# Performance work log

Hardware: AMD Instinct MI355X
Metric: run time of the kernel (lower is better)

The kernel has to match this reference:

```python
import jax, jax.numpy as jnp
import numpy as np

B, N, F_IN, K, OUT = 64, 512, 6, 8, 3
SLOPE = 0.01  # torch LeakyReLU default negative_slope


def lrelu(x):
    return jnp.where(x >= 0, x, SLOPE * x)


def edge_mlp(e, w1, b1, w2, b2):
    # Linear -> LeakyReLU -> Linear -> LeakyReLU (EdgeConvMLP / mlp1)
    return lrelu(lrelu(e @ w1 + b1) @ w2 + b2)


def dyn_edge_conv(x, w1, b1, w2, b2):
    # x: [B, N, F]. kNN in feature space within each graph (self included,
    # matching torch_cluster.knn used by PyG DynamicEdgeConv).
    x2 = jnp.sum(x * x, -1)                                   # [B, N]
    d = x2[:, :, None] + x2[:, None, :] - 2.0 * jnp.einsum('bnf,bmf->bnm', x, x)
    idx = jax.lax.top_k(-d, K)[1]                              # [B, N, K]
    xj = jax.vmap(lambda xb, ib: xb[ib])(x, idx)               # [B, N, K, F]
    xi = jnp.broadcast_to(x[:, :, None, :], xj.shape)
    e = jnp.concatenate([xi, xj - xi], -1)                     # [B, N, K, 2F]
    h = edge_mlp(e, w1, b1, w2, b2)                            # [B, N, K, 256]
    return h.max(axis=2)                                       # max aggregation


def _lin(key, din, dout):
    kw, kb = jax.random.split(key)
    s = 1.0 / np.sqrt(din)
    w = jax.random.uniform(kw, (din, dout), jnp.float32, -s, s)
    b = jax.random.uniform(kb, (dout,), jnp.float32, -s, s)
    return w, b


def setup_inputs() -> dict:
    key = jax.random.key(0)
    ks = jax.random.split(key, 20)
    inp = {}
    inp['x'] = jax.random.normal(ks[0], (B * N, F_IN), jnp.float32)
    inp['edge_index'] = jax.random.randint(ks[1], (2, B * N * K), 0, B * N, jnp.int64)  # unused
    inp['batch'] = jnp.repeat(jnp.arange(B, dtype=jnp.int64), N)
    dims = [(2 * F_IN, 336, 256), (512, 336, 256), (512, 336, 256), (512, 336, 256)]
    for i, (din, dh, do) in enumerate(dims):
        w1, b1 = _lin(ks[2 + 2 * i], din, dh)
        w2, b2 = _lin(ks[3 + 2 * i], dh, do)
        inp[f'c{i+1}_w1'], inp[f'c{i+1}_b1'] = w1, b1
        inp[f'c{i+1}_w2'], inp[f'c{i+1}_b2'] = w2, b2
    inp['m1_w1'], inp['m1_b1'] = _lin(ks[10], 256 * 4 + F_IN, 336)
    inp['m1_w2'], inp['m1_b2'] = _lin(ks[11], 336, 256)
    inp['m2_w1'], inp['m2_b1'] = _lin(ks[12], 256, 128)
    inp['m2_w2'], inp['m2_b2'] = _lin(ks[13], 128, OUT)
    return inp


def reference(x, edge_index, batch,
              c1_w1, c1_b1, c1_w2, c1_b2,
              c2_w1, c2_b1, c2_w2, c2_b2,
              c3_w1, c3_b1, c3_w2, c3_b2,
              c4_w1, c4_b1, c4_w2, c4_b2,
              m1_w1, m1_b1, m1_w2, m1_b2,
              m2_w1, m2_b1, m2_w2, m2_b2):
    # edge_index is unused: DynamicEdgeConv rebuilds the kNN graph each layer.
    # Equal-sized graphs: reshape instead of segment ops (batch = repeat(arange(B), N)).
    xb = x.reshape(B, N, F_IN)
    x1 = dyn_edge_conv(xb, c1_w1, c1_b1, c1_w2, c1_b2)
    x2 = dyn_edge_conv(x1, c2_w1, c2_b1, c2_w2, c2_b2)
    x3 = dyn_edge_conv(x2, c3_w1, c3_b1, c3_w2, c3_b2)
    x4 = dyn_edge_conv(x3, c4_w1, c4_b1, c4_w2, c4_b2)
    h = jnp.concatenate([xb, x1, x2, x3, x4], -1)   # [B, N, 1030]
    h = edge_mlp(h, m1_w1, m1_b1, m1_w2, m1_b2)     # [B, N, 256]
    g = h.mean(axis=1)                              # global_mean_pool -> [B, 256]
    return lrelu(g @ m2_w1 + m2_b1) @ m2_w2 + m2_b2  # [B, OUT]
```

## Files before the change

### kernel.cpp

```cpp
#include <hip/hip_runtime.h>
#include <hip/hip_bf16.h>


#define DEVFN __device__ __forceinline__
DEVFN float lrelu(float v) { return v >= 0.f ? v : 0.01f * v; }

using bf16x8 = __attribute__((ext_vector_type(8))) short;
using f32x4  = __attribute__((ext_vector_type(4))) float;

template<int N> struct IC { static constexpr int value = N; };

DEVFN unsigned short f2bf(float v) {
    __hip_bfloat16 h = __float2bfloat16(v);
    return *(unsigned short*)&h;
}
DEVFN float bf2f(unsigned short u) {
    return __uint_as_float((unsigned)u << 16);
}

struct PDesc { const float* src; unsigned short* dst; int Kt, NT, N, mode, p0, p1, Ksrc; };
struct PTable { PDesc d[13]; };

__global__ __launch_bounds__(256) void pack_kernel(PTable tb) {
    PDesc d = tb.d[blockIdx.y];
    int i = blockIdx.x * 256 + threadIdx.x;
    int tot = d.Kt * d.NT * 512;
    if (i >= tot) return;
    int j = i & 7, lane = (i >> 3) & 63;
    int tile = i >> 9;
    int nt = tile % d.NT, kt = tile / d.NT;
    int k = kt * 32 + ((lane >> 4) << 3) + j;
    int n = nt * 16 + (lane & 15);
    float v = 0.f;
    if (d.mode == 0) {
        if (k < d.Ksrc) v = d.src[(size_t)k * d.N + n];
    } else if (d.mode == 1) {
        if (k < d.p1) v = d.src[(size_t)k * d.N + n] - d.src[(size_t)(k + d.p1) * d.N + n];
        else if (k >= d.p0 && k < d.p0 + d.p1) v = d.src[(size_t)(k - d.p0 + d.p1) * d.N + n];
    } else if (d.mode == 2) {
        if (k < 6) v = d.src[(size_t)k * d.N + n];
        else if (k >= 32 && k < 1056) v = d.src[(size_t)(k - 26) * d.N + n];
    } else {
        v = d.src[(size_t)(k + d.p0) * d.N + n];
    }
    d.dst[i] = f2bf(v);
}

__global__ __launch_bounds__(256) void xbprep_kernel(const float* __restrict__ xb,
                                                     unsigned short* __restrict__ xbbf,
                                                     unsigned short* __restrict__ xcat) {
    int p = blockIdx.x * 256 + threadIdx.x;
    if (p >= 32768) return;
    unsigned short r[16];
    #pragma unroll
    for (int c = 0; c < 6; ++c) r[c] = f2bf(xb[p * 6 + c]);
    #pragma unroll
    for (int c = 6; c < 16; ++c) r[c] = 0;
    #pragma unroll
    for (int c = 0; c < 16; ++c) xbbf[p * 16 + c] = r[c];
    unsigned short* xc = xcat + (size_t)p * 1056;
    #pragma unroll
    for (int c = 0; c < 16; ++c) xc[c] = r[c];
    #pragma unroll
    for (int c = 16; c < 32; ++c) xc[c] = 0;
}

template<int F>
__global__ __launch_bounds__(256) void norms_kernel(const float* __restrict__ f,
                                                    float* __restrict__ nrm) {
    int p = blockIdx.x * 256 + threadIdx.x;
    if (p >= 64 * 512) return;
    const float* r = f + (size_t)p * F;
    float s = 0.f;
    #pragma unroll
    for (int i = 0; i < F; ++i) s += r[i] * r[i];
    nrm[p] = s;
}

template<int F>
__global__ __launch_bounds__(256) void knn_kernel(const float* __restrict__ feat,
                                                  const float* __restrict__ nrm,
                                                  int* __restrict__ knn) {
    constexpr int FP = (F == 6) ? 8 : (F + 4);
    __shared__ float Xq[32 * FP];
    __shared__ float Xc[32 * FP];
    __shared__ float qn[32], cn[32];
    __shared__ float dt[32 * 33];
    const int t  = threadIdx.x;
    const int b  = blockIdx.x >> 4;
    const int n0 = (blockIdx.x & 15) << 5;
    const float* fg = feat + (size_t)b * 512 * F;

    for (int i = t; i < 32 * F; i += 256) {
        int r = i / F, c = i - r * F;
        Xq[r * FP + c] = fg[(size_t)(n0 + r) * F + c];
    }
    if (t < 32) qn[t] = nrm[b * 512 + n0 + t];

    float d8[8]; int i8[8];
    #pragma unroll
    for (int k = 0; k < 8; ++k) { d8[k] = 3.4e38f; i8[k] = 0; }

    const int q = t >> 3, cs = t & 7;

    for (int ct = 0; ct < 16; ++ct) {
        const int c0 = ct << 5;
        __syncthreads();
        for (int i = t; i < 32 * F; i += 256) {
            int r = i / F, c = i - r * F;
            Xc[r * FP + c] = fg[(size_t)(c0 + r) * F + c];
        }
        if (t < 32) cn[t] = nrm[b * 512 + c0 + t];
        __syncthreads();

        float acc[4] = {0.f, 0.f, 0.f, 0.f};
        #pragma unroll
        for (int f = 0; f < F; ++f) {
            float qv = Xq[q * FP + f];
            #pragma unroll
            for (int j = 0; j < 4; ++j) acc[j] += qv * Xc[(cs + 8 * j) * FP + f];
        }
        #pragma unroll
        for (int j = 0; j < 4; ++j)
            dt[q * 33 + cs + 8 * j] = qn[q] + cn[cs + 8 * j] - 2.f * acc[j];
        __syncthreads();

        if (t < 32) {
            #pragma unroll 1
            for (int i = 0; i < 32; ++i) {
                float d = dt[t * 33 + i];
                if (d < d8[7]) {
                    d8[7] = d; i8[7] = c0 + i;
                    #pragma unroll
                    for (int s = 7; s >= 1; --s) {
                        if (d8[s] < d8[s - 1]) {
                            float td = d8[s]; d8[s] = d8[s - 1]; d8[s - 1] = td;
                            int   ti = i8[s]; i8[s] = i8[s - 1]; i8[s - 1] = ti;
                        }
                    }
                }
            }
        }
    }
    if (t < 32) {
        #pragma unroll
        for (int k = 0; k < 8; ++k)
            knn[((size_t)b * 512 + n0 + t) * 8 + k] = i8[k];
    }
}

__global__ __launch_bounds__(256, 2)
void knn_mfma(const unsigned short* __restrict__ xfl,
              const float* __restrict__ nrm,
              int* __restrict__ knn) {
    __shared__ unsigned short Qh[64 * 72], Ql[64 * 72], Ch[64 * 72], Cl[64 * 72];
    __shared__ float dt[64 * 66];
    __shared__ float qn[64], cn[64];
    float* mD = dt;
    int*   mI = (int*)(dt + 2048);

    const int t  = threadIdx.x;
    const int l  = t & 63, w = t >> 6;
    const int m16 = l & 15, q4 = l >> 4;
    const int bx = blockIdx.x;
    const int slot = bx >> 3;
    const int b  = (bx & 7) + 8 * (slot >> 3);
    const int qs = (slot & 7) << 6;

    if (t < 64) qn[t] = nrm[b * 512 + qs + t];

    float d8[8]; int i8[8];
    #pragma unroll
    for (int k = 0; k < 8; ++k) { d8[k] = 3.4e38f; i8[k] = 0x7fffffff; }

    const int sr = t >> 2;
    const int sc = (t & 3) << 4;
    const int tq = t & 63, sub = t >> 6;

    for (int cs = 0; cs < 8; ++cs) {
        const int c0 = cs << 6;
        if (t < 64) cn[t] = nrm[b * 512 + c0 + t];

        f32x4 acc[4];
        #pragma unroll
        for (int i = 0; i < 4; ++i) acc[i] = (f32x4){0.f, 0.f, 0.f, 0.f};

        for (int kc = 0; kc < 4; ++kc) {
            const int k0 = kc << 6;
            __syncthreads();
            {
                const unsigned short* qr = xfl + (size_t)(b * 512 + qs + sr) * 512;
                const unsigned short* cr = xfl + (size_t)(b * 512 + c0 + sr) * 512;
                *(uint4*)&Qh[sr * 72 + sc]     = *(const uint4*)(qr + k0 + sc);
                *(uint4*)&Qh[sr * 72 + sc + 8] = *(const uint4*)(qr + k0 + sc + 8);
                *(uint4*)&Ql[sr * 72 + sc]     = *(const uint4*)(qr + 256 + k0 + sc);
                *(uint4*)&Ql[sr * 72 + sc + 8] = *(const uint4*)(qr + 256 + k0 + sc + 8);
                *(uint4*)&Ch[sr * 72 + sc]     = *(const uint4*)(cr + k0 + sc);
                *(uint4*)&Ch[sr * 72 + sc + 8] = *(const uint4*)(cr + k0 + sc + 8);
                *(uint4*)&Cl[sr * 72 + sc]     = *(const uint4*)(cr + 256 + k0 + sc);
                *(uint4*)&Cl[sr * 72 + sc + 8] = *(const uint4*)(cr + 256 + k0 + sc + 8);
            }
            __syncthreads();

            #pragma unroll
            for (int kt = 0; kt < 2; ++kt) {
                const int ko = kt * 32 + q4 * 8;
                bf16x8 ah = *(const bf16x8*)&Qh[(w * 16 + m16) * 72 + ko];
                bf16x8 al = *(const bf16x8*)&Ql[(w * 16 + m16) * 72 + ko];
                #pragma unroll
                for (int nt = 0; nt < 4; ++nt) {
                    bf16x8 bh = *(const bf16x8*)&Ch[(nt * 16 + m16) * 72 + ko];
                    bf16x8 bl = *(const bf16x8*)&Cl[(nt * 16 + m16) * 72 + ko];
                    acc[nt] = __builtin_amdgcn_mfma_f32_16x16x32_bf16(ah, bh, acc[nt], 0, 0, 0);
                    acc[nt] = __builtin_amdgcn_mfma_f32_16x16x32_bf16(ah, bl, acc[nt], 0, 0, 0);
                    acc[nt] = __builtin_amdgcn_mfma_f32_16x16x32_bf16(al, bh, acc[nt], 0, 0, 0);
                }
            }
        }

        #pragma unroll
        for (int nt = 0; nt < 4; ++nt) {
            float cv = cn[nt * 16 + m16];
            #pragma unroll
            for (int rr = 0; rr < 4; ++rr) {
                int qr = w * 16 + q4 * 4 + rr;
                dt[qr * 66 + nt * 16 + m16] = qn[qr] + cv - 2.f * acc[nt][rr];
            }
        }
        __syncthreads();

        {
            const float* drow = &dt[tq * 66 + sub * 16];
            #pragma unroll 1
            for (int j = 0; j < 16; ++j) {
                float d = drow[j];
                if (d < d8[7]) {
                    d8[7] = d; i8[7] = c0 + sub * 16 + j;
                    #pragma unroll
                    for (int s = 7; s >= 1; --s) {
                        if (d8[s] < d8[s - 1]) {
                            float td = d8[s]; d8[s] = d8[s - 1]; d8[s - 1] = td;
                            int   ti = i8[s]; i8[s] = i8[s - 1]; i8[s - 1] = ti;
                        }
                    }
                }
            }
        }
        __syncthreads();
    }

    #pragma unroll
    for (int k = 0; k < 8; ++k) {
        mD[(tq * 4 + sub) * 8 + k] = d8[k];
        mI[(tq * 4 + sub) * 8 + k] = i8[k];
    }
    __syncthreads();
    if (t < 64) {
        int p[4] = {0, 0, 0, 0};
        int outb = (b * 512 + qs + t) * 8;
        #pragma unroll 1
        for (int k = 0; k < 8; ++k) {
            float bd = 3.5e38f; int bi = 0x7fffffff; int bs = 0;
            #pragma unroll
            for (int s = 0; s < 4; ++s) {
                if (p[s] < 8) {
                    float dd = mD[(t * 4 + s) * 8 + p[s]];
                    int   ii = mI[(t * 4 + s) * 8 + p[s]];
                    if (dd < bd || (dd == bd && ii < bi)) { bd = dd; bi = ii; bs = s; }
                }
            }
            knn[outb + k] = bi;
            p[bs]++;
        }
    }
}

__global__ __launch_bounds__(256, 2)
void pgemm_kernel(const unsigned short* __restrict__ xfl,
                  const unsigned short* __restrict__ Wa,
                  const unsigned short* __restrict__ Wb,
                  const float* __restrict__ B1,
                  unsigned short* __restrict__ Pa,
                  unsigned short* __restrict__ Pb) {
    __shared__ unsigned short smem[64 * 344];
    const int t = threadIdx.x;
    const int l = t & 63, w = t >> 6;
    const int q4 = l >> 4, m16 = l & 15;
    const int s1 = w * 6;
    const int bx = blockIdx.x & 511;
    const bool isA = !(blockIdx.x & 512);
    const unsigned short* W1ap = isA ? Wa : Wb;
    unsigned short*       Pp   = isA ? Pa : Pb;
    const int slot = bx >> 3;
    const int r0 = ((bx & 7) + 8 * (slot >> 3)) * 512 + (slot & 7) * 64;

    {
        const int r = t >> 2;
        const unsigned short* srow = xfl + (size_t)(r0 + r) * 512;
        #pragma unroll
        for (int s = 0; s < 8; ++s) {
            int c16 = (t & 3) + (s << 2);
            *(uint4*)&smem[r * 264 + c16 * 8] = *(const uint4*)(srow + c16 * 8);
        }
    }
    __syncthreads();

    f32x4 acc[4][6];
    #pragma unroll
    for (int mt = 0; mt < 4; ++mt)
        #pragma unroll
        for (int n = 0; n < 6; ++n) acc[mt][n] = (f32x4){0.f, 0.f, 0.f, 0.f};

    auto run = [&](auto c1c) {
        constexpr int C1 = decltype(c1c)::value;
        bf16x8 bcur[C1];
        {
            const unsigned short* bp = W1ap + ((size_t)s1 * 64 + l) * 8;
            #pragma unroll
            for (int n = 0; n < C1; ++n) bcur[n] = *(const bf16x8*)(bp + n * 512);
        }
        #pragma unroll 1
        for (int kt = 0; kt < 8; ++kt) {
            bf16x8 bnext[C1];
            if (kt + 1 < 8) {
                const unsigned short* bp = W1ap + ((size_t)((kt + 1) * 21 + s1) * 64 + l) * 8;
                #pragma unroll
                for (int n = 0; n < C1; ++n) bnext[n] = *(const bf16x8*)(bp + n * 512);
            }
            bf16x8 af[4];
            #pragma unroll
            for (int mt = 0; mt < 4; ++mt)
                af[mt] = *(const bf16x8*)&smem[(mt * 16 + m16) * 264 + q4 * 8 + kt * 32];
            #pragma unroll
            for (int n = 0; n < C1; ++n)
                #pragma unroll
                for (int mt = 0; mt < 4; ++mt)
                    acc[mt][n] = __builtin_amdgcn_mfma_f32_16x16x32_bf16(af[mt], bcur[n], acc[mt][n], 0, 0, 0);
            #pragma unroll
            for (int n = 0; n < C1; ++n) bcur[n] = bnext[n];
        }
    };
    if (w < 3) run(IC<6>{});
    else       run(IC<3>{});

    __syncthreads();
    {
        const int c1 = (w < 3) ? 6 : 3;
        for (int n = 0; n < c1; ++n) {
            int col = (s1 + n) * 16 + m16;
            float bias = isA ? B1[col] : 0.f;
            #pragma unroll
            for (int mt = 0; mt < 4; ++mt)
                #pragma unroll
                for (int r = 0; r < 4; ++r)
                    smem[(mt * 16 + q4 * 4 + r) * 344 + col] = f2bf(acc[mt][n][r] + bias);
        }
    }
    __syncthreads();
    {
        uint4* dst = (uint4*)(Pp + (size_t)r0 * 336);
        const uint4* src = (const uint4*)smem;
        #pragma unroll 1
        for (int i = t; i < 2688; i += 256)
            dst[i] = src[(i / 42) * 43 + (i % 42)];
    }
}

template<int MODE>
__global__ __launch_bounds__(256, 3)
void mfma_mlp(const unsigned short* __restrict__ featbf,
              const int* __restrict__ knn,
              const unsigned short* __restrict__ W1p, const float* __restrict__ B1,
              const unsigned short* __restrict__ W2p, const float* __restrict__ B2,
              const unsigned short* __restrict__ Pp,
              const unsigned short* __restrict__ Pbp,
              float* __restrict__ outf,
              unsigned short* __restrict__ xcat, int sliceoff,
              unsigned short* __restrict__ xfl, float* __restrict__ nrm) {
    constexpr int NCHUNK  = (MODE == 2) ? 3 : 1;
    constexpr int KTPC    = (MODE == 1) ? 1 : 11;
    constexpr int ASTRIDE = (MODE == 1) ? 40 : 360;

    __shared__ unsigned short smem[64 * 360];
    __shared__ int rowi[64];
    __shared__ int rowj[64];
    __shared__ float nparts[8][4];

    const int t = threadIdx.x;
    const int l = t & 63, w = t >> 6;
    const int q4 = l >> 4, m16 = l & 15;
    const int s1 = w * 6;
    const int s2 = w * 4;

    const int bx = blockIdx.x;
    int p0;
    if constexpr (MODE != 2) {
        int slot = bx >> 3;
        int g = (bx & 7) + 8 * (slot >> 6);
        p0 = g * 512 + (slot & 63) * 8;
    } else {
        int slot = bx >> 3;
        int g = (bx & 7) + 8 * (slot >> 3);
        p0 = g * 512 + (slot & 7) * 64;
    }

    if (MODE != 2 && t < 64) {
        int pt = p0 + (t >> 3);
        rowi[t] = pt;
        rowj[t] = (pt & ~511) + knn[pt * 8 + (t & 7)];
    }

    if constexpr (MODE == 3) {
        __syncthreads();
        const int row = t >> 2;
        const int u0  = t & 3;
        const unsigned short* va = Pp  + (size_t)rowi[row] * 336;
        const unsigned short* vb = Pbp + (size_t)rowj[row] * 336;
        uint4 A[11], Bv[11];
        #pragma unroll
        for (int k = 0; k < 11; ++k) {
            int u = u0 + 4 * k;
            if (u < 42) {
                A[k]  = *(const uint4*)(va + u * 8);
                Bv[k] = *(const uint4*)(vb + u * 8);
            }
        }
        #pragma unroll
        for (int k = 0; k < 11; ++k) {
            int u = u0 + 4 * k;
            if (u < 42) {
                const unsigned short* sa = (const unsigned short*)&A[k];
                const unsigned short* sb = (const unsigned short*)&Bv[k];
                uint4 ov;
                unsigned short* o = (unsigned short*)&ov;
                #pragma unroll
                for (int j = 0; j < 8; ++j)
                    o[j] = f2bf(lrelu(bf2f(sa[j]) + bf2f(sb[j])));
                *(uint4*)&smem[row * 360 + u * 8] = ov;
            }
        }
    } else {
        f32x4 acc1[4][6];
        #pragma unroll
        for (int mt = 0; mt < 4; ++mt)
            #pragma unroll
            for (int n = 0; n < 6; ++n) acc1[mt][n] = (f32x4){0.f, 0.f, 0.f, 0.f};

        auto g1 = [&](auto c1c, int ktbase) {
            constexpr int C1 = decltype(c1c)::value;
            bf16x8 bcur[C1];
            {
                const unsigned short* bp =
                    W1p + ((size_t)(ktbase * 21 + s1) * 64 + l) * 8;
                #pragma unroll
                for (int n = 0; n < C1; ++n) bcur[n] = *(const bf16x8*)(bp + n * 512);
            }
            #pragma unroll 1
            for (int kt = 0; kt < KTPC; ++kt) {
                bf16x8 bnext[C1];
                if (kt + 1 < KTPC) {
                    const unsigned short* bp =
                        W1p + ((size_t)((ktbase + kt + 1) * 21 + s1) * 64 + l) * 8;
                    #pragma unroll
                    for (int n = 0; n < C1; ++n) bnext[n] = *(const bf16x8*)(bp + n * 512);
                }
                bf16x8 af[4];
                #pragma unroll
                for (int mt = 0; mt < 4; ++mt)
                    af[mt] = *(const bf16x8*)&smem[(mt * 16 + m16) * ASTRIDE + q4 * 8 + kt * 32];
                #pragma unroll
                for (int n = 0; n < C1; ++n)
                    #pragma unroll
                    for (int mt = 0; mt < 4; ++mt)
                        acc1[mt][n] = __builtin_amdgcn_mfma_f32_16x16x32_bf16(af[mt], bcur[n], acc1[mt][n], 0, 0, 0);
                #pragma unroll
                for (int n = 0; n < C1; ++n) bcur[n] = bnext[n];
            }
        };

        for (int kc = 0; kc < NCHUNK; ++kc) {
            __syncthreads();
            if constexpr (MODE == 1) {
                const int r = t >> 2, c16 = t & 3;
                const unsigned short* s2p =
                    featbf + (size_t)(c16 < 2 ? rowi[r] : rowj[r]) * 16 + (c16 & 1) * 8;
                *(uint4*)&smem[r * 40 + c16 * 8] = *(const uint4*)s2p;
            } else {
                const int r = t >> 2;
                const unsigned short* srow =
                    featbf + (size_t)(p0 + r) * 1056 + kc * 352;
                #pragma unroll
                for (int s = 0; s < 11; ++s) {
                    int c16 = (t & 3) + (s << 2);
                    *(uint4*)&smem[r * 360 + c16 * 8] = *(const uint4*)(srow + c16 * 8);
                }
            }
            __syncthreads();

            if (w < 3) g1(IC<6>{}, kc * KTPC);
            else       g1(IC<3>{}, kc * KTPC);
        }
        __syncthreads();

        {
            const int c1 = (w < 3) ? 6 : 3;
            for (int n = 0; n < c1; ++n) {
                int nt = s1 + n;
                float b = B1[nt * 16 + m16];
                #pragma unroll
                for (int mt = 0; mt < 4; ++mt) {
                    #pragma unroll
                    for (int r = 0; r < 4; ++r) {
                        int row = mt * 16 + q4 * 4 + r;
                        float v = acc1[mt][n][r] + b;
                        smem[row * 360 + nt * 16 + m16] = f2bf(lrelu(v));
                    }
                }
            }
        }
    }

    if (t < 64) {
        #pragma unroll
        for (int c = 336; c < 352; ++c) smem[t * 360 + c] = 0;
    }
    __syncthreads();

    f32x4 acc2[4][4];
    #pragma unroll
    for (int mt = 0; mt < 4; ++mt)
        #pragma unroll
        for (int n = 0; n < 4; ++n) acc2[mt][n] = (f32x4){0.f, 0.f, 0.f, 0.f};
    {
        bf16x8 b0[4], b1f[4];
        {
            const unsigned short* bp0 = W2p + ((size_t)s2 * 64 + l) * 8;
            const unsigned short* bp1 = W2p + ((size_t)(16 + s2) * 64 + l) * 8;
            #pragma unroll
            for (int n = 0; n < 4; ++n) {
                b0[n]  = *(const bf16x8*)(bp0 + n * 512);
                b1f[n] = *(const bf16x8*)(bp1 + n * 512);
            }
        }
        #pragma unroll 1
        for (int kt = 0; kt < 11; ++kt) {
            bf16x8 b2[4];
            if (kt + 2 < 11) {
                const unsigned short* bp = W2p + ((size_t)((kt + 2) * 16 + s2) * 64 + l) * 8;
                #pragma unroll
                for (int n = 0; n < 4; ++n) b2[n] = *(const bf16x8*)(bp + n * 512);
            }
            bf16x8 af[4];
            #pragma unroll
            for (int mt = 0; mt < 4; ++mt)
                af[mt] = *(const bf16x8*)&smem[(mt * 16 + m16) * 360 + q4 * 8 + kt * 32];
            #pragma unroll
            for (int n = 0; n < 4; ++n)
                #pragma unroll
                for (int mt = 0; mt < 4; ++mt)
                    acc2[mt][n] = __builtin_amdgcn_mfma_f32_16x16x32_bf16(af[mt], b0[n], acc2[mt][n], 0, 0, 0);
            #pragma unroll
            for (int n = 0; n < 4; ++n) { b0[n] = b1f[n]; b1f[n] = b2[n]; }
        }
    }

    if constexpr (MODE != 2) {
        __syncthreads();
        unsigned short* sh = smem;
        #pragma unroll
        for (int mt = 0; mt < 4; ++mt) {
            float nsum = 0.f;
            int plocal = mt * 2 + (q4 >> 1);
            #pragma unroll
            for (int n = 0; n < 4; ++n) {
                int nt = s2 + n;
                float b = B2[nt * 16 + m16];
                float mv = -3.4e38f;
                #pragma unroll
                for (int r = 0; r < 4; ++r) mv = fmaxf(mv, lrelu(acc2[mt][n][r] + b));
                mv = fmaxf(mv, __shfl_xor(mv, 16, 64));
                if ((q4 & 1) == 0) {
                    int col = nt * 16 + m16;
                    unsigned short hi = f2bf(mv);
                    float fhi = bf2f(hi);
                    unsigned short lo = f2bf(mv - fhi);
                    float xr = fhi + bf2f(lo);
                    nsum += xr * xr;
                    sh[plocal * 512 + col] = hi;
                    sh[plocal * 512 + 256 + col] = lo;
                }
            }
            #pragma unroll
            for (int o = 1; o < 16; o <<= 1) nsum += __shfl_xor(nsum, o, 64);
            if ((q4 & 1) == 0 && m16 == 0) nparts[plocal][w] = nsum;
        }
        __syncthreads();
        {
            int r = t >> 5, cb = (t & 31) * 16;
            int p = p0 + r;
            uint4 v0 = *(uint4*)&sh[r * 512 + cb];
            uint4 v1 = *(uint4*)&sh[r * 512 + cb + 8];
            *(uint4*)&xfl[(size_t)p * 512 + cb]     = v0;
            *(uint4*)&xfl[(size_t)p * 512 + cb + 8] = v1;
            if (cb < 256) {
                *(uint4*)&xcat[(size_t)p * 1056 + sliceoff + cb]     = v0;
                *(uint4*)&xcat[(size_t)p * 1056 + sliceoff + cb + 8] = v1;
            }
        }
        if (t < 8)
            nrm[p0 + t] =
                nparts[t][0] + nparts[t][1] + nparts[t][2] + nparts[t][3];
    } else {
        #pragma unroll
        for (int mt = 0; mt < 4; ++mt)
            #pragma unroll
            for (int n = 0; n < 4; ++n) {
                int nt = s2 + n;
                float b = B2[nt * 16 + m16];
                int col = nt * 16 + m16;
                #pragma unroll
                for (int r = 0; r < 4; ++r) {
                    int p = p0 + mt * 16 + q4 * 4 + r;
                    outf[(size_t)p * 256 + col] = lrelu(acc2[mt][n][r] + b);
                }
            }
    }
}

__global__ __launch_bounds__(256) void pool_kernel(const float* __restrict__ h,
                                                   float* __restrict__ g) {
    int b = blockIdx.x, t = threadIdx.x;
    const float* hb = h + (size_t)b * 512 * 256;
    float s = 0.f;
    for (int n = 0; n < 512; ++n) s += hb[n * 256 + t];
    g[b * 256 + t] = s * (1.f / 512.f);
}

__global__ __launch_bounds__(128) void head_kernel(const float* __restrict__ g,
                                                   const float* __restrict__ w1,
                                                   const float* __restrict__ b1,
                                                   const float* __restrict__ w2,
                                                   const float* __restrict__ b2,
                                                   float* __restrict__ out) {
    __shared__ float gs[256];
    __shared__ float hid[128];
    int b = blockIdx.x, t = threadIdx.x;
    gs[t] = g[b * 256 + t];
    gs[t + 128] = g[b * 256 + t + 128];
    __syncthreads();
    float s = b1[t];
    for (int c = 0; c < 256; ++c) s += gs[c] * w1[c * 128 + t];
    hid[t] = lrelu(s);
    __syncthreads();
    if (t < 3) {
        float o = b2[t];
        for (int j = 0; j < 128; ++j) o += hid[j] * w2[j * 3 + t];
        out[b * 3 + t] = o;
    }
}

extern "C" void kernel_launch(void* const* d_in, const int* in_sizes, int n_in,
                              void* d_out, int out_size, void* d_ws, size_t ws_size,
                              hipStream_t stream) {
    const float* xb = (const float*)d_in[0];
    const float* c_w1[4] = { (const float*)d_in[3],  (const float*)d_in[7],
                             (const float*)d_in[11], (const float*)d_in[15] };
    const float* c_b1[4] = { (const float*)d_in[4],  (const float*)d_in[8],
                             (const float*)d_in[12], (const float*)d_in[16] };
    const float* c_w2[4] = { (const float*)d_in[5],  (const float*)d_in[9],
                             (const float*)d_in[13], (const float*)d_in[17] };
    const float* c_b2[4] = { (const float*)d_in[6],  (const float*)d_in[10],
                             (const float*)d_in[14], (const float*)d_in[18] };
    const float* m1w1 = (const float*)d_in[19];
    const float* m1b1 = (const float*)d_in[20];
    const float* m1w2 = (const float*)d_in[21];
    const float* m1b2 = (const float*)d_in[22];
    const float* m2w1 = (const float*)d_in[23];
    const float* m2b1 = (const float*)d_in[24];
    const float* m2w2 = (const float*)d_in[25];
    const float* m2b2 = (const float*)d_in[26];

    char* base = (char*)d_ws;
    size_t off = 0;
    auto alloc = [&](size_t bytes) { char* p = base + off; off = (off + bytes + 255) & ~(size_t)255; return p; };
    int*            knn   = (int*)           alloc((size_t)32768 * 8 * 4);
    float*          nrm   = (float*)         alloc((size_t)32768 * 4);
    char*           Preg  =                  alloc((size_t)32768 * 256 * 4);
    unsigned short* Ppb   = (unsigned short*)alloc((size_t)32768 * 336 * 2);
    float*          g     = (float*)         alloc(64 * 256 * 4);
    unsigned short* xcat  = (unsigned short*)alloc((size_t)32768 * 1056 * 2);
    unsigned short* xfl   = (unsigned short*)alloc((size_t)32768 * 512 * 2);
    unsigned short* xbbf  = (unsigned short*)alloc((size_t)32768 * 16 * 2);
    unsigned short* w1p1  = (unsigned short*)alloc((size_t)1  * 21 * 512 * 2);
    unsigned short* w2p1  = (unsigned short*)alloc((size_t)11 * 16 * 512 * 2);
    unsigned short* w1a[3]; unsigned short* w1b[3]; unsigned short* w2p[3];
    for (int i = 0; i < 3; ++i) {
        w1a[i] = (unsigned short*)alloc((size_t)8  * 21 * 512 * 2);
        w1b[i] = (unsigned short*)alloc((size_t)8  * 21 * 512 * 2);
        w2p[i] = (unsigned short*)alloc((size_t)11 * 16 * 512 * 2);
    }
    unsigned short* m1p1  = (unsigned short*)alloc((size_t)33 * 21 * 512 * 2);
    unsigned short* m1p2  = (unsigned short*)alloc((size_t)11 * 16 * 512 * 2);
    unsigned short* Pp = (unsigned short*)Preg;
    float*          hm = (float*)Preg;

    PTable tb;
    tb.d[0] = { c_w1[0], w1p1, 1,  21, 336, 1, 16,  6,   0   };
    tb.d[1] = { c_w2[0], w2p1, 11, 16, 256, 0, 0,   0,   336 };
    for (int i = 0; i < 3; ++i) {
        tb.d[2 + 3 * i] = { c_w1[i + 1], w1a[i], 8,  21, 336, 1, 0,   256, 0   };
        tb.d[3 + 3 * i] = { c_w1[i + 1], w1b[i], 8,  21, 336, 3, 256, 0,   0   };
        tb.d[4 + 3 * i] = { c_w2[i + 1], w2p[i], 11, 16, 256, 0, 0,   0,   336 };
    }
    tb.d[11] = { m1w1, m1p1, 33, 21, 336, 2, 0, 0, 0   };
    tb.d[12] = { m1w2, m1p2, 11, 16, 256, 0, 0, 0, 336 };
    pack_kernel<<<dim3(1386, 13), dim3(256), 0, stream>>>(tb);
    xbprep_kernel<<<128, 256, 0, stream>>>(xb, xbbf, xcat);

    norms_kernel<6><<<128, 256, 0, stream>>>(xb, nrm);
    knn_kernel<6><<<1024, 256, 0, stream>>>(xb, nrm, knn);
    mfma_mlp<1><<<4096, 256, 0, stream>>>(xbbf, knn,
                                          w1p1, c_b1[0], w2p1, c_b2[0], nullptr, nullptr,
                                          nullptr, xcat, 32, xfl, nrm);

    for (int l = 1; l < 4; ++l) {
        int dstslice = 32 + l * 256;
        knn_mfma<<<512, 256, 0, stream>>>(xfl, nrm, knn);
        pgemm_kernel<<<1024, 256, 0, stream>>>(xfl, w1a[l - 1], w1b[l - 1], c_b1[l], Pp, Ppb);
        mfma_mlp<3><<<4096, 256, 0, stream>>>(nullptr, knn,
                                              nullptr, nullptr, w2p[l - 1], c_b2[l], Pp, Ppb,
                                              nullptr, xcat, dstslice, xfl, nrm);
    }

    mfma_mlp<2><<<512, 256, 0, stream>>>(xcat, nullptr,
                                         m1p1, m1b1, m1p2, m1b2, nullptr, nullptr,
                                         hm, nullptr, 0, nullptr, nullptr);

    pool_kernel<<<64, 256, 0, stream>>>(hm, g);
    head_kernel<<<64, 128, 0, stream>>>(g, m2w1, m2b1, m2w2, m2b2, (float*)d_out);
}
```

Before: 1.049 ms.

## Add dedicated register-resident conv kernel for layers 2-4 edge MLP second GEMM

Replaces the MODE 3 path of mfma_mlp with a new conv_fused kernel. Each wave holds the gathered and activated hidden edge features directly in registers as MFMA A operands, which avoids the shared-memory staging round trip. Each wave then computes all 256 output columns for 16 edges, with W2 fragments streamed straight from global memory. The max over neighbours is done with a lane shuffle, and the norm and hi/lo bf16 outputs are written through a small shared buffer. Each wave now reloads the full W2 matrix from global/L2, and the accumulator array raises register pressure.

```diff
diff --git a/kernel.cpp b/kernel.cpp
--- a/kernel.cpp
+++ b/kernel.cpp
@@ -366,14 +366,124 @@
     }
 }
 
+__global__ __launch_bounds__(256, 3)
+void conv_fused(const int* __restrict__ knn,
+                const unsigned short* __restrict__ Pab,
+                const unsigned short* __restrict__ Pbp,
+                const unsigned short* __restrict__ W2p,
+                const float* __restrict__ B2,
+                unsigned short* __restrict__ xcat, int sliceoff,
+                unsigned short* __restrict__ xfl, float* __restrict__ nrm) {
+    __shared__ unsigned short sh[8 * 512];
+    __shared__ int rowi[64], rowj[64];
+
+    const int t = threadIdx.x;
+    const int l = t & 63, w = t >> 6;
+    const int q4 = l >> 4, m16 = l & 15;
+
+    const int bx = blockIdx.x;
+    const int slot = bx >> 3;
+    const int g = (bx & 7) + 8 * (slot >> 6);
+    const int p0 = g * 512 + (slot & 63) * 8;
+
+    if (t < 64) {
+        int pt = p0 + (t >> 3);
+        rowi[t] = pt;
+        rowj[t] = (pt & ~511) + knn[pt * 8 + (t & 7)];
+    }
+    __syncthreads();
+
+    const int e = w * 16 + m16;
+    const unsigned short* va = Pab + (size_t)rowi[e] * 336;
+    const unsigned short* vb = Pbp + (size_t)rowj[e] * 336;
+
+    uint4 ra[11], rb[11];
+    #pragma unroll
+    for (int kt = 0; kt < 11; ++kt) {
+        int c0 = kt * 32 + q4 * 8;
+        if (kt < 10 || q4 < 2) {
+            ra[kt] = *(const uint4*)(va + c0);
+            rb[kt] = *(const uint4*)(vb + c0);
+        }
+    }
+    bf16x8 A[11];
+    #pragma unroll
+    for (int kt = 0; kt < 11; ++kt) {
+        if (kt < 10 || q4 < 2) {
+            const unsigned short* sa = (const unsigned short*)&ra[kt];
+            const unsigned short* sb = (const unsigned short*)&rb[kt];
+            bf16x8 av;
+            #pragma unroll
+            for (int j = 0; j < 8; ++j)
+                av[j] = (short)f2bf(lrelu(bf2f(sa[j]) + bf2f(sb[j])));
+            A[kt] = av;
+        } else {
+            A[kt] = (bf16x8){0, 0, 0, 0, 0, 0, 0, 0};
+        }
+    }
+
+    f32x4 acc[16];
+    #pragma unroll
+    for (int n = 0; n < 16; ++n) acc[n] = (f32x4){0.f, 0.f, 0.f, 0.f};
+
+    #pragma unroll
+    for (int np = 0; np < 8; ++np) {
+        const int n0 = np * 2, n1 = np * 2 + 1;
+        #pragma unroll
+        for (int kt = 0; kt < 11; ++kt) {
+            bf16x8 b0 = *(const bf16x8*)(W2p + ((size_t)(kt * 16 + n0) * 64 + l) * 8);
+            bf16x8 b1 = *(const bf16x8*)(W2p + ((size_t)(kt * 16 + n1) * 64 + l) * 8);
+            acc[n0] = __builtin_amdgcn_mfma_f32_16x16x32_bf16(A[kt], b0, acc[n0], 0, 0, 0);
+            acc[n1] = __builtin_amdgcn_mfma_f32_16x16x32_bf16(A[kt], b1, acc[n1], 0, 0, 0);
+        }
+    }
+
+    {
+        const int plocal = w * 2 + (q4 >> 1);
+        float nsum = 0.f;
+        #pragma unroll
+        for (int n = 0; n < 16; ++n) {
+            int col = n * 16 + m16;
+            float b = B2[col];
+            float mv = -3.4e38f;
+            #pragma unroll
+            for (int r = 0; r < 4; ++r) mv = fmaxf(mv, lrelu(acc[n][r] + b));
+            mv = fmaxf(mv, __shfl_xor(mv, 16, 64));
+            if ((q4 & 1) == 0) {
+                unsigned short hi = f2bf(mv);
+                float fhi = bf2f(hi);
+                unsigned short lo = f2bf(mv - fhi);
+                float xr = fhi + bf2f(lo);
+                nsum += xr * xr;
+                sh[plocal * 512 + col] = hi;
+                sh[plocal * 512 + 256 + col] = lo;
+            }
+        }
+        #pragma unroll
+        for (int o = 1; o < 16; o <<= 1) nsum += __shfl_xor(nsum, o, 64);
+        if ((q4 & 1) == 0 && m16 == 0) nrm[p0 + plocal] = nsum;
+    }
+    __syncthreads();
+    {
+        int r = t >> 5, cb = (t & 31) * 16;
+        int p = p0 + r;
+        uint4 v0 = *(uint4*)&sh[r * 512 + cb];
+        uint4 v1 = *(uint4*)&sh[r * 512 + cb + 8];
+        *(uint4*)&xfl[(size_t)p * 512 + cb]     = v0;
+        *(uint4*)&xfl[(size_t)p * 512 + cb + 8] = v1;
+        if (cb < 256) {
+            *(uint4*)&xcat[(size_t)p * 1056 + sliceoff + cb]     = v0;
+            *(uint4*)&xcat[(size_t)p * 1056 + sliceoff + cb + 8] = v1;
+        }
+    }
+}
+
 template<int MODE>
 __global__ __launch_bounds__(256, 3)
 void mfma_mlp(const unsigned short* __restrict__ featbf,
               const int* __restrict__ knn,
               const unsigned short* __restrict__ W1p, const float* __restrict__ B1,
               const unsigned short* __restrict__ W2p, const float* __restrict__ B2,
-              const unsigned short* __restrict__ Pp,
-              const unsigned short* __restrict__ Pbp,
               float* __restrict__ outf,
               unsigned short* __restrict__ xcat, int sliceoff,
               unsigned short* __restrict__ xfl, float* __restrict__ nrm) {
@@ -410,111 +520,80 @@
         rowj[t] = (pt & ~511) + knn[pt * 8 + (t & 7)];
     }
 
-    if constexpr (MODE == 3) {
+    f32x4 acc1[4][6];
+    #pragma unroll
+    for (int mt = 0; mt < 4; ++mt)
+        #pragma unroll
+        for (int n = 0; n < 6; ++n) acc1[mt][n] = (f32x4){0.f, 0.f, 0.f, 0.f};
+
+    auto g1 = [&](auto c1c, int ktbase) {
+        constexpr int C1 = decltype(c1c)::value;
+        bf16x8 bcur[C1];
+        {
+            const unsigned short* bp =
+                W1p + ((size_t)(ktbase * 21 + s1) * 64 + l) * 8;
+            #pragma unroll
+            for (int n = 0; n < C1; ++n) bcur[n] = *(const bf16x8*)(bp + n * 512);
+        }
+        #pragma unroll 1
+        for (int kt = 0; kt < KTPC; ++kt) {
+            bf16x8 bnext[C1];
+            if (kt + 1 < KTPC) {
+                const unsigned short* bp =
+                    W1p + ((size_t)((ktbase + kt + 1) * 21 + s1) * 64 + l) * 8;
+                #pragma unroll
+                for (int n = 0; n < C1; ++n) bnext[n] = *(const bf16x8*)(bp + n * 512);
+            }
+            bf16x8 af[4];
+            #pragma unroll
+            for (int mt = 0; mt < 4; ++mt)
+                af[mt] = *(const bf16x8*)&smem[(mt * 16 + m16) * ASTRIDE + q4 * 8 + kt * 32];
+            #pragma unroll
+            for (int n = 0; n < C1; ++n)
+                #pragma unroll
+                for (int mt = 0; mt < 4; ++mt)
+                    acc1[mt][n] = __builtin_amdgcn_mfma_f32_16x16x32_bf16(af[mt], bcur[n], acc1[mt][n], 0, 0, 0);
+            #pragma unroll
+            for (int n = 0; n < C1; ++n) bcur[n] = bnext[n];
+        }
+    };
+
+    for (int kc = 0; kc < NCHUNK; ++kc) {
         __syncthreads();
-        const int row = t >> 2;
-        const int u0  = t & 3;
-        const unsigned short* va = Pp  + (size_t)rowi[row] * 336;
-        const unsigned short* vb = Pbp + (size_t)rowj[row] * 336;
-        uint4 A[11], Bv[11];
-        #pragma unroll
-        for (int k = 0; k < 11; ++k) {
-            int u = u0 + 4 * k;
-            if (u < 42) {
-                A[k]  = *(const uint4*)(va + u * 8);
-                Bv[k] = *(const uint4*)(vb + u * 8);
-            }
-        }
-        #pragma unroll
-        for (int k = 0; k < 11; ++k) {
-            int u = u0 + 4 * k;
-            if (u < 42) {
-                const unsigned short* sa = (const unsigned short*)&A[k];
-                const unsigned short* sb = (const unsigned short*)&Bv[k];
-                uint4 ov;
-                unsigned short* o = (unsigned short*)&ov;
-                #pragma unroll
-                for (int j = 0; j < 8; ++j)
-                    o[j] = f2bf(lrelu(bf2f(sa[j]) + bf2f(sb[j])));
-                *(uint4*)&smem[row * 360 + u * 8] = ov;
-            }
-        }
-    } else {
-        f32x4 acc1[4][6];
-        #pragma unroll
-        for (int mt = 0; mt < 4; ++mt)
-            #pragma unroll
-            for (int n = 0; n < 6; ++n) acc1[mt][n] = (f32x4){0.f, 0.f, 0.f, 0.f};
-
-        auto g1 = [&](auto c1c, int ktbase) {
-            constexpr int C1 = decltype(c1c)::value;
-            bf16x8 bcur[C1];
-            {
-                const unsigned short* bp =
-                    W1p + ((size_t)(ktbase * 21 + s1) * 64 + l) * 8;
-                #pragma unroll
-                for (int n = 0; n < C1; ++n) bcur[n] = *(const bf16x8*)(bp + n * 512);
-            }
-            #pragma unroll 1
-            for (int kt = 0; kt < KTPC; ++kt) {
-                bf16x8 bnext[C1];
-                if (kt + 1 < KTPC) {
-                    const unsigned short* bp =
-                        W1p + ((size_t)((ktbase + kt + 1) * 21 + s1) * 64 + l) * 8;
-                    #pragma unroll
-                    for (int n = 0; n < C1; ++n) bnext[n] = *(const bf16x8*)(bp + n * 512);
-                }
-                bf16x8 af[4];
-                #pragma unroll
-                for (int mt = 0; mt < 4; ++mt)
-                    af[mt] = *(const bf16x8*)&smem[(mt * 16 + m16) * ASTRIDE + q4 * 8 + kt * 32];
-                #pragma unroll
-                for (int n = 0; n < C1; ++n)
-                    #pragma unroll
-                    for (int mt = 0; mt < 4; ++mt)
-                        acc1[mt][n] = __builtin_amdgcn_mfma_f32_16x16x32_bf16(af[mt], bcur[n], acc1[mt][n], 0, 0, 0);
-                #pragma unroll
-                for (int n = 0; n < C1; ++n) bcur[n] = bnext[n];
-            }
-        };
-
-        for (int kc = 0; kc < NCHUNK; ++kc) {
-            __syncthreads();
-            if constexpr (MODE == 1) {
-                const int r = t >> 2, c16 = t & 3;
-                const unsigned short* s2p =
-                    featbf + (size_t)(c16 < 2 ? rowi[r] : rowj[r]) * 16 + (c16 & 1) * 8;
-                *(uint4*)&smem[r * 40 + c16 * 8] = *(const uint4*)s2p;
-            } else {
-                const int r = t >> 2;
-                const unsigned short* srow =
-                    featbf + (size_t)(p0 + r) * 1056 + kc * 352;
-                #pragma unroll
-                for (int s = 0; s < 11; ++s) {
-                    int c16 = (t & 3) + (s << 2);
-                    *(uint4*)&smem[r * 360 + c16 * 8] = *(const uint4*)(srow + c16 * 8);
-                }
-            }
-            __syncthreads();
-
-            if (w < 3) g1(IC<6>{}, kc * KTPC);
-            else       g1(IC<3>{}, kc * KTPC);
+        if constexpr (MODE == 1) {
+            const int r = t >> 2, c16 = t & 3;
+            const unsigned short* s2p =
+                featbf + (size_t)(c16 < 2 ? rowi[r] : rowj[r]) * 16 + (c16 & 1) * 8;
+            *(uint4*)&smem[r * 40 + c16 * 8] = *(const uint4*)s2p;
+        } else {
+            const int r = t >> 2;
+            const unsigned short* srow =
+                featbf + (size_t)(p0 + r) * 1056 + kc * 352;
+            #pragma unroll
+            for (int s = 0; s < 11; ++s) {
+                int c16 = (t & 3) + (s << 2);
+                *(uint4*)&smem[r * 360 + c16 * 8] = *(const uint4*)(srow + c16 * 8);
+            }
         }
         __syncthreads();
 
-        {
-            const int c1 = (w < 3) ? 6 : 3;
-            for (int n = 0; n < c1; ++n) {
-                int nt = s1 + n;
-                float b = B1[nt * 16 + m16];
-                #pragma unroll
-                for (int mt = 0; mt < 4; ++mt) {
-                    #pragma unroll
-                    for (int r = 0; r < 4; ++r) {
-                        int row = mt * 16 + q4 * 4 + r;
-                        float v = acc1[mt][n][r] + b;
-                        smem[row * 360 + nt * 16 + m16] = f2bf(lrelu(v));
-                    }
+        if (w < 3) g1(IC<6>{}, kc * KTPC);
+        else       g1(IC<3>{}, kc * KTPC);
+    }
+    __syncthreads();
+
+    {
+        const int c1 = (w < 3) ? 6 : 3;
+        for (int n = 0; n < c1; ++n) {
+            int nt = s1 + n;
+            float b = B1[nt * 16 + m16];
+            #pragma unroll
+            for (int mt = 0; mt < 4; ++mt) {
+                #pragma unroll
+                for (int r = 0; r < 4; ++r) {
+                    int row = mt * 16 + q4 * 4 + r;
+                    float v = acc1[mt][n][r] + b;
+                    smem[row * 360 + nt * 16 + m16] = f2bf(lrelu(v));
                 }
             }
         }
@@ -720,20 +799,19 @@
     norms_kernel<6><<<128, 256, 0, stream>>>(xb, nrm);
     knn_kernel<6><<<1024, 256, 0, stream>>>(xb, nrm, knn);
     mfma_mlp<1><<<4096, 256, 0, stream>>>(xbbf, knn,
-                                          w1p1, c_b1[0], w2p1, c_b2[0], nullptr, nullptr,
+                                          w1p1, c_b1[0], w2p1, c_b2[0],
                                           nullptr, xcat, 32, xfl, nrm);
 
     for (int l = 1; l < 4; ++l) {
         int dstslice = 32 + l * 256;
         knn_mfma<<<512, 256, 0, stream>>>(xfl, nrm, knn);
         pgemm_kernel<<<1024, 256, 0, stream>>>(xfl, w1a[l - 1], w1b[l - 1], c_b1[l], Pp, Ppb);
-        mfma_mlp<3><<<4096, 256, 0, stream>>>(nullptr, knn,
-                                              nullptr, nullptr, w2p[l - 1], c_b2[l], Pp, Ppb,
-                                              nullptr, xcat, dstslice, xfl, nrm);
+        conv_fused<<<4096, 256, 0, stream>>>(knn, Pp, Ppb, w2p[l - 1], c_b2[l],
+                                             xcat, dstslice, xfl, nrm);
     }
 
     mfma_mlp<2><<<512, 256, 0, stream>>>(xcat, nullptr,
-                                         m1p1, m1b1, m1p2, m1b2, nullptr, nullptr,
+                                         m1p1, m1b1, m1p2, m1b2,
                                          hm, nullptr, 0, nullptr, nullptr);
 
     pool_kernel<<<64, 256, 0, stream>>>(hm, g);
```

New measurement: 1.250 ms. +19.2%, slower.
